# Performance work log

Measured on AMD Instinct MI355X. Metric: run time of the kernel, lower is better.

The kernel has to match this reference:

```python
import jax, jax.numpy as jnp
import numpy as np

B, P, L = 8, 196, 80
DIM1, DIM2, ATT = 2048, 300, 1024


def setup_inputs() -> dict:
    key = jax.random.key(0)
    ks = jax.random.split(key, 8)
    s1 = 1.0 / np.sqrt(DIM1)
    s2 = 1.0 / np.sqrt(DIM2)
    sa = 1.0 / np.sqrt(ATT)
    return {
        "x1": jax.random.normal(ks[0], (B, P, DIM1), jnp.float32),
        "x2": jax.random.normal(ks[1], (B, L, DIM2), jnp.float32),
        "W1": jax.random.uniform(ks[2], (ATT, DIM1), jnp.float32, -s1, s1),
        "W2": jax.random.uniform(ks[3], (ATT, DIM2), jnp.float32, -s2, s2),
        "Wh": jax.random.uniform(ks[4], (ATT, ATT), jnp.float32, -sa, sa),
        "bh": jax.random.uniform(ks[5], (ATT,), jnp.float32, -sa, sa),
        "wt": jax.random.uniform(ks[6], (ATT,), jnp.float32, -sa, sa),
        "bt": jax.random.uniform(ks[7], (), jnp.float32, -sa, sa),
    }


def reference(x1, x2, W1, W2, Wh, bh, wt, bt):
    # project: p1 (B,P,A), p2 (B,L,A)
    p1 = jnp.einsum("bpd,ad->bpa", x1, W1)
    p2 = jnp.einsum("bld,ad->bla", x2, W2)
    # broadcast bilinear + tanh: (B,L,P,A)
    h = jnp.tanh(p1[:, None, :, :] * p2[:, :, None, :])
    # hidden linear then target linear (rank-1 on last dim)
    t = jnp.einsum("blpa,ca->blpc", h, Wh) + bh
    alpha = jnp.einsum("blpc,c->blp", t, wt) + bt  # (B,L,P)
    return alpha
```

## Files before the change

### kernel.cpp

```cpp
#include <hip/hip_runtime.h>
#include <hip/hip_bf16.h>

static constexpr int kB   = 8;
static constexpr int kP   = 196;
static constexpr int kL   = 80;
static constexpr int kD1  = 2048;
static constexpr int kD2  = 300;
static constexpr int kD2p = 320;
static constexpr int kATT = 1024;
static constexpr int kM   = kB * kP;
static constexpr int kR2  = kB * kL;
static constexpr int kOut = kB * kL * kP;
static constexpr int kASplit = 16;
static constexpr int kAChunk = kATT / kASplit;
static constexpr int kLPer   = 5;

static constexpr float kTanhScale = 2.8853900817779268f;

__device__ __forceinline__ unsigned short f2bf(float x) {
    union { float f; unsigned int u; } c; c.f = x;
    unsigned int r = c.u + 0x7fffu + ((c.u >> 16) & 1u);
    return (unsigned short)(r >> 16);
}

typedef __attribute__((ext_vector_type(8))) short  bf16x8;
typedef __attribute__((ext_vector_type(4))) float  f32x4;

__device__ __forceinline__ void load_lds16(const void* g, void* l) {
    __builtin_amdgcn_global_load_lds(
        (const __attribute__((address_space(1))) void*)g,
        (__attribute__((address_space(3))) void*)l, 16, 0, 0);
}

static constexpr int kN4a = kM * kD1 / 4;
static constexpr int kN4b = kATT * kD1 / 4;
static constexpr int kN1  = kR2 * kD2p;
static constexpr int kN2  = kATT * kD2p;
static constexpr int kCastBlocks =
    (kN4a + kN4b + kN1 + kN2 + 255) / 256;

__global__ __launch_bounds__(256) void prep_kernel(
        const float* __restrict__ x1, unsigned short* __restrict__ x1b,
        const float* __restrict__ W1, unsigned short* __restrict__ W1b,
        const float* __restrict__ x2, unsigned short* __restrict__ x2b,
        const float* __restrict__ W2, unsigned short* __restrict__ W2b,
        const float* __restrict__ Wh, const float* __restrict__ wt,
        const float* __restrict__ bh, const float* __restrict__ bt,
        float* __restrict__ v, float* __restrict__ beta) {
    if (blockIdx.x >= kCastBlocks) {
        int bid = blockIdx.x - kCastBlocks;
        int ax  = bid & 3;
        int c0  = (bid >> 2) * 64;
        int a   = ax * 256 + threadIdx.x;
        float acc = 0.0f;
        #pragma unroll 8
        for (int c = c0; c < c0 + 64; ++c)
            acc = fmaf(wt[c], Wh[(size_t)c * kATT + a], acc);
        atomicAdd(&v[a], acc);
        if (ax == 0 && threadIdx.x < 64) {
            int c = c0 + threadIdx.x;
            float pb = wt[c] * bh[c];
            #pragma unroll
            for (int off = 32; off > 0; off >>= 1)
                pb += __shfl_down(pb, off, 64);
            if (threadIdx.x == 0) {
                if (c0 == 0) pb += bt[0];
                atomicAdd(beta, pb);
            }
        }
        return;
    }
    int i = blockIdx.x * 256 + threadIdx.x;
    if (i < kN4a) {
        float4 f = ((const float4*)x1)[i];
        ushort4 o = { f2bf(f.x), f2bf(f.y), f2bf(f.z), f2bf(f.w) };
        ((ushort4*)x1b)[i] = o;
    } else if ((i -= kN4a) < kN4b) {
        float4 f = ((const float4*)W1)[i];
        ushort4 o = { f2bf(f.x), f2bf(f.y), f2bf(f.z), f2bf(f.w) };
        ((ushort4*)W1b)[i] = o;
    } else if ((i -= kN4b) < kN1) {
        int r = i / kD2p, c = i - r * kD2p;
        x2b[i] = (c < kD2) ? f2bf(x2[(size_t)r * kD2 + c]) : (unsigned short)0;
    } else if ((i -= kN1) < kN2) {
        int r = i / kD2p, c = i - r * kD2p;
        W2b[i] = (c < kD2) ? f2bf(W2[(size_t)r * kD2 + c]) : (unsigned short)0;
    }
}

static constexpr int kP2Blocks = (kR2 / 64) * (kATT / 64);
static constexpr int kP1Blocks = ((kM + 63) / 64) * (kATT / 64);

__global__ __launch_bounds__(256) void gemm_all_kernel(
        const unsigned short* __restrict__ x2b, const unsigned short* __restrict__ W2b,
        float* __restrict__ p2w,
        const unsigned short* __restrict__ x1b, const unsigned short* __restrict__ W1b,
        float* __restrict__ p1w) {
    __shared__ unsigned short As[64 * 64];
    __shared__ unsigned short Bs[64 * 64];

    const unsigned short *Ab, *Bb;
    float* Co; int M, K, mx, nx; float scale;
    {
        int bid = blockIdx.x;
        if (bid < kP2Blocks) {
            Ab = x2b; Bb = W2b; Co = p2w; M = kR2; K = kD2p; scale = 1.0f;
            mx = bid % (kR2 / 64); nx = bid / (kR2 / 64);
        } else {
            int l = bid - kP2Blocks;
            Ab = x1b; Bb = W1b; Co = p1w; M = kM; K = kD1; scale = kTanhScale;
            mx = l % ((kM + 63) / 64); nx = l / ((kM + 63) / 64);
        }
    }
    const int m0   = mx * 64;
    const int n0   = nx * 64;
    const int tid  = threadIdx.x;
    const int lane = tid & 63;
    const int wv   = tid >> 6;
    const int mh   = (wv >> 1) * 32;
    const int nh   = (wv & 1) * 32;

    const int row0 = tid >> 3;
    const int row1 = row0 + 32;
    const int kx   = ((tid & 7) ^ (row0 & 7)) * 8;
    const int ar0 = min(m0 + row0, M - 1), ar1 = min(m0 + row1, M - 1);
    const int br0 = n0 + row0,             br1 = n0 + row1;

    f32x4 acc[2][2] = {};
    for (int k0 = 0; k0 < K; k0 += 64) {
        load_lds16(Ab + (size_t)ar0 * K + k0 + kx, (char*)As + tid * 16);
        load_lds16(Ab + (size_t)ar1 * K + k0 + kx, (char*)As + (tid + 256) * 16);
        load_lds16(Bb + (size_t)br0 * K + k0 + kx, (char*)Bs + tid * 16);
        load_lds16(Bb + (size_t)br1 * K + k0 + kx, (char*)Bs + (tid + 256) * 16);
        __syncthreads();

        #pragma unroll
        for (int kk = 0; kk < 2; ++kk) {
            bf16x8 af[2], bf[2];
            #pragma unroll
            for (int i = 0; i < 2; ++i) {
                int r   = mh + i * 16 + (lane & 15);
                int col = (kk * 64 + (lane >> 4) * 16) ^ ((r & 7) << 4);
                af[i] = *(const bf16x8*)((const char*)As + r * 128 + col);
            }
            #pragma unroll
            for (int j = 0; j < 2; ++j) {
                int r   = nh + j * 16 + (lane & 15);
                int col = (kk * 64 + (lane >> 4) * 16) ^ ((r & 7) << 4);
                bf[j] = *(const bf16x8*)((const char*)Bs + r * 128 + col);
            }
            #pragma unroll
            for (int i = 0; i < 2; ++i)
                #pragma unroll
                for (int j = 0; j < 2; ++j)
                    acc[i][j] = __builtin_amdgcn_mfma_f32_16x16x32_bf16(
                                    af[i], bf[j], acc[i][j], 0, 0, 0);
        }
        __syncthreads();
    }

    #pragma unroll
    for (int i = 0; i < 2; ++i)
        #pragma unroll
        for (int j = 0; j < 2; ++j)
            #pragma unroll
            for (int r = 0; r < 4; ++r) {
                int m = m0 + mh + i * 16 + (lane >> 4) * 4 + r;
                int n = n0 + nh + j * 16 + (lane & 15);
                if (m < M) Co[(size_t)m * kATT + n] = scale * acc[i][j][r];
            }
}

__global__ __launch_bounds__(256) void alpha_kernel(
        const float* __restrict__ p1, const float* __restrict__ p2,
        const float* __restrict__ v, float* __restrict__ part) {
    __shared__ float vs[kAChunk];
    __shared__ float sred;
    const int b     = blockIdx.y;
    const int as    = blockIdx.z;
    const int aBase = as * kAChunk;
    const int p0    = blockIdx.x * 16;
    const int tid   = threadIdx.x;
    const int tp    = tid & 15;
    const int lg    = tid >> 4;

    if (tid < kAChunk) vs[tid] = v[aBase + tid];
    __syncthreads();
    if (tid < 64) {
        float s = vs[tid & (kAChunk - 1)] * ((tid < kAChunk) ? 1.0f : 0.0f);
        s = vs[tid < kAChunk ? tid : 0];
        if (tid >= kAChunk) s = 0.0f;
        #pragma unroll
        for (int off = 32; off > 0; off >>= 1)
            s += __shfl_down(s, off, 64);
        if (tid == 0) sred = s;
    }
    __syncthreads();
    const float sumV = sred;

    const int p   = p0 + tp;
    const int gr1 = b * kP + min(p, kP - 1);
    const float* pu = p1 + (size_t)gr1 * kATT + aBase;
    const float* pw = p2 + ((size_t)(b * kL + lg * kLPer)) * kATT + aBase;

    float acc[kLPer] = {};
    #pragma unroll 2
    for (int a4 = 0; a4 < kAChunk / 4; ++a4) {
        float4 u  = *(const float4*)(pu + a4 * 4);
        float4 vv = *(const float4*)&vs[a4 * 4];
        #pragma unroll
        for (int j = 0; j < kLPer; ++j) {
            float4 w = *(const float4*)(pw + (size_t)j * kATT + a4 * 4);
            acc[j] = fmaf(vv.x, __builtin_amdgcn_rcpf(__builtin_amdgcn_exp2f(u.x * w.x) + 1.0f), acc[j]);
            acc[j] = fmaf(vv.y, __builtin_amdgcn_rcpf(__builtin_amdgcn_exp2f(u.y * w.y) + 1.0f), acc[j]);
            acc[j] = fmaf(vv.z, __builtin_amdgcn_rcpf(__builtin_amdgcn_exp2f(u.z * w.z) + 1.0f), acc[j]);
            acc[j] = fmaf(vv.w, __builtin_amdgcn_rcpf(__builtin_amdgcn_exp2f(u.w * w.w) + 1.0f), acc[j]);
        }
    }
    if (p < kP) {
        float* po = part + (size_t)as * kOut + ((size_t)b * kL + lg * kLPer) * kP + p;
        #pragma unroll
        for (int j = 0; j < kLPer; ++j)
            po[(size_t)j * kP] = sumV - 2.0f * acc[j];
    }
}

__global__ __launch_bounds__(256) void reduce_kernel(
        const float* __restrict__ part, const float* __restrict__ beta,
        float* __restrict__ out) {
    int i = blockIdx.x * 256 + threadIdx.x;
    if (i < kOut) {
        float s = beta[0];
        #pragma unroll
        for (int r = 0; r < kASplit; ++r)
            s += part[(size_t)r * kOut + i];
        out[i] = s;
    }
}

extern "C" void kernel_launch(void* const* d_in, const int* in_sizes, int n_in,
                              void* d_out, int out_size, void* d_ws, size_t ws_size,
                              hipStream_t stream) {
    const float* x1 = (const float*)d_in[0];
    const float* x2 = (const float*)d_in[1];
    const float* W1 = (const float*)d_in[2];
    const float* W2 = (const float*)d_in[3];
    const float* Wh = (const float*)d_in[4];
    const float* bh = (const float*)d_in[5];
    const float* wt = (const float*)d_in[6];
    const float* bt = (const float*)d_in[7];
    float* out = (float*)d_out;

    float* ws   = (float*)d_ws;
    float* v    = ws;
    float* beta = ws + 1024;
    float* p2w  = ws + 1088;
    float* p1w  = p2w + (size_t)kR2 * kATT;
    unsigned short* x1b = (unsigned short*)(p1w + (size_t)kM * kATT);
    unsigned short* W1b = x1b + (size_t)kM * kD1;
    unsigned short* x2b = W1b + (size_t)kATT * kD1;
    unsigned short* W2b = x2b + (size_t)kR2 * kD2p;
    float* part = (float*)(W2b + (size_t)kATT * kD2p);

    hipMemsetAsync(ws, 0, 1088 * sizeof(float), stream);

    prep_kernel<<<dim3(kCastBlocks + 64), 256, 0, stream>>>(
        x1, x1b, W1, W1b, x2, x2b, W2, W2b, Wh, wt, bh, bt, v, beta);
    gemm_all_kernel<<<dim3(kP2Blocks + kP1Blocks), 256, 0, stream>>>(
        x2b, W2b, p2w, x1b, W1b, p1w);
    alpha_kernel<<<dim3((kP + 15) / 16, kB, kASplit), 256, 0, stream>>>(
        p1w, p2w, v, part);
    reduce_kernel<<<dim3((kOut + 255) / 256), 256, 0, stream>>>(part, beta, out);
}
```

Baseline: 148.4 us.

## Use 128x128 split-K double-buffered P1 GEMM and atomic output accumulation

The large x1·W1 projection now uses 128x128 tiles with a 2-way K split and double-buffered LDS prefetch, writing two partial buffers that alpha_kernel sums on load. The reduce kernel and partial buffer are gone: the GEMM launch also initialises the output with beta, and alpha_kernel atomically adds its per-chunk contributions. The v/beta precompute drops the memset and atomics in favour of full per-thread loops over only 4 blocks. Trade-offs are more LDS per block, extra p1 reads in alpha, float atomic contention on the output, and a long serial loop in the v computation.

```diff
diff --git a/kernel.cpp b/kernel.cpp
--- a/kernel.cpp
+++ b/kernel.cpp
@@ -49,24 +49,21 @@
         float* __restrict__ v, float* __restrict__ beta) {
     if (blockIdx.x >= kCastBlocks) {
         int bid = blockIdx.x - kCastBlocks;
-        int ax  = bid & 3;
-        int c0  = (bid >> 2) * 64;
-        int a   = ax * 256 + threadIdx.x;
+        int a   = bid * 256 + threadIdx.x;
         float acc = 0.0f;
         #pragma unroll 8
-        for (int c = c0; c < c0 + 64; ++c)
+        for (int c = 0; c < kATT; ++c)
             acc = fmaf(wt[c], Wh[(size_t)c * kATT + a], acc);
-        atomicAdd(&v[a], acc);
-        if (ax == 0 && threadIdx.x < 64) {
-            int c = c0 + threadIdx.x;
-            float pb = wt[c] * bh[c];
+        v[a] = acc;
+        if (bid == 0 && threadIdx.x < 64) {
+            float pb = 0.0f;
+            #pragma unroll 4
+            for (int c = threadIdx.x; c < kATT; c += 64)
+                pb = fmaf(wt[c], bh[c], pb);
             #pragma unroll
             for (int off = 32; off > 0; off >>= 1)
                 pb += __shfl_down(pb, off, 64);
-            if (threadIdx.x == 0) {
-                if (c0 == 0) pb += bt[0];
-                atomicAdd(beta, pb);
-            }
+            if (threadIdx.x == 0) beta[0] = pb + bt[0];
         }
         return;
     }
@@ -88,92 +85,180 @@
     }
 }
 
-static constexpr int kP2Blocks = (kR2 / 64) * (kATT / 64);
-static constexpr int kP1Blocks = ((kM + 63) / 64) * (kATT / 64);
+static constexpr int kP1Mt      = (kM + 127) / 128;
+static constexpr int kP1Blocks  = kP1Mt * (kATT / 128) * 2;
+static constexpr int kP2Blocks  = (kR2 / 64) * (kATT / 64);
+static constexpr int kInitBlocks = (kOut + 255) / 256;
+static constexpr int kKHalf     = kD1 / 2;
 
 __global__ __launch_bounds__(256) void gemm_all_kernel(
         const unsigned short* __restrict__ x2b, const unsigned short* __restrict__ W2b,
         float* __restrict__ p2w,
         const unsigned short* __restrict__ x1b, const unsigned short* __restrict__ W1b,
-        float* __restrict__ p1w) {
-    __shared__ unsigned short As[64 * 64];
-    __shared__ unsigned short Bs[64 * 64];
-
-    const unsigned short *Ab, *Bb;
-    float* Co; int M, K, mx, nx; float scale;
-    {
-        int bid = blockIdx.x;
-        if (bid < kP2Blocks) {
-            Ab = x2b; Bb = W2b; Co = p2w; M = kR2; K = kD2p; scale = 1.0f;
-            mx = bid % (kR2 / 64); nx = bid / (kR2 / 64);
-        } else {
-            int l = bid - kP2Blocks;
-            Ab = x1b; Bb = W1b; Co = p1w; M = kM; K = kD1; scale = kTanhScale;
-            mx = l % ((kM + 63) / 64); nx = l / ((kM + 63) / 64);
-        }
-    }
-    const int m0   = mx * 64;
-    const int n0   = nx * 64;
+        float* __restrict__ p1a, float* __restrict__ p1b,
+        const float* __restrict__ beta, float* __restrict__ outp) {
+    __shared__ unsigned short As2[2][128 * 64];
+    __shared__ unsigned short Bs2[2][128 * 64];
+
+    const int bid  = blockIdx.x;
     const int tid  = threadIdx.x;
     const int lane = tid & 63;
     const int wv   = tid >> 6;
-    const int mh   = (wv >> 1) * 32;
-    const int nh   = (wv & 1) * 32;
-
-    const int row0 = tid >> 3;
-    const int row1 = row0 + 32;
-    const int kx   = ((tid & 7) ^ (row0 & 7)) * 8;
-    const int ar0 = min(m0 + row0, M - 1), ar1 = min(m0 + row1, M - 1);
-    const int br0 = n0 + row0,             br1 = n0 + row1;
-
-    f32x4 acc[2][2] = {};
-    for (int k0 = 0; k0 < K; k0 += 64) {
-        load_lds16(Ab + (size_t)ar0 * K + k0 + kx, (char*)As + tid * 16);
-        load_lds16(Ab + (size_t)ar1 * K + k0 + kx, (char*)As + (tid + 256) * 16);
-        load_lds16(Bb + (size_t)br0 * K + k0 + kx, (char*)Bs + tid * 16);
-        load_lds16(Bb + (size_t)br1 * K + k0 + kx, (char*)Bs + (tid + 256) * 16);
+
+    if (bid >= kP1Blocks + kP2Blocks) {
+        int i = (bid - kP1Blocks - kP2Blocks) * 256 + tid;
+        if (i < kOut) outp[i] = beta[0];
+        return;
+    }
+
+    if (bid < kP1Blocks) {
+        const int l  = bid;
+        const int ks = l & 1;
+        const int t  = l >> 1;
+        const int mx = t % kP1Mt, nx = t / kP1Mt;
+        const int m0 = mx * 128, n0 = nx * 128;
+        const int kBeg = ks * kKHalf;
+
+        const int srow = tid >> 3;
+        const int kx   = ((tid & 7) ^ (srow & 7)) * 8;
+        int ar[4], br[4];
+        #pragma unroll
+        for (int q = 0; q < 4; ++q) {
+            ar[q] = min(m0 + srow + q * 32, kM - 1);
+            br[q] = n0 + srow + q * 32;
+        }
+        const int wr = (wv >> 1) * 64;
+        const int wc = (wv & 1) * 64;
+
+        f32x4 acc[4][4] = {};
+
+        #pragma unroll
+        for (int q = 0; q < 4; ++q) {
+            load_lds16(x1b + (size_t)ar[q] * kD1 + kBeg + kx,
+                       (char*)As2[0] + (tid + q * 256) * 16);
+            load_lds16(W1b + (size_t)br[q] * kD1 + kBeg + kx,
+                       (char*)Bs2[0] + (tid + q * 256) * 16);
+        }
         __syncthreads();
 
-        #pragma unroll
-        for (int kk = 0; kk < 2; ++kk) {
-            bf16x8 af[2], bf[2];
-            #pragma unroll
-            for (int i = 0; i < 2; ++i) {
-                int r   = mh + i * 16 + (lane & 15);
-                int col = (kk * 64 + (lane >> 4) * 16) ^ ((r & 7) << 4);
-                af[i] = *(const bf16x8*)((const char*)As + r * 128 + col);
+        int buf = 0;
+        for (int k0 = 0; k0 < kKHalf; k0 += 64) {
+            if (k0 + 64 < kKHalf) {
+                const int kp = kBeg + k0 + 64;
+                #pragma unroll
+                for (int q = 0; q < 4; ++q) {
+                    load_lds16(x1b + (size_t)ar[q] * kD1 + kp + kx,
+                               (char*)As2[buf ^ 1] + (tid + q * 256) * 16);
+                    load_lds16(W1b + (size_t)br[q] * kD1 + kp + kx,
+                               (char*)Bs2[buf ^ 1] + (tid + q * 256) * 16);
+                }
             }
-            #pragma unroll
-            for (int j = 0; j < 2; ++j) {
-                int r   = nh + j * 16 + (lane & 15);
-                int col = (kk * 64 + (lane >> 4) * 16) ^ ((r & 7) << 4);
-                bf[j] = *(const bf16x8*)((const char*)Bs + r * 128 + col);
+            const char* Ap = (const char*)As2[buf];
+            const char* Bp = (const char*)Bs2[buf];
+            #pragma unroll
+            for (int kk = 0; kk < 2; ++kk) {
+                bf16x8 af[4], bf[4];
+                #pragma unroll
+                for (int i = 0; i < 4; ++i) {
+                    int r   = wr + i * 16 + (lane & 15);
+                    int col = (kk * 64 + (lane >> 4) * 16) ^ ((r & 7) << 4);
+                    af[i] = *(const bf16x8*)(Ap + r * 128 + col);
+                }
+                #pragma unroll
+                for (int j = 0; j < 4; ++j) {
+                    int r   = wc + j * 16 + (lane & 15);
+                    int col = (kk * 64 + (lane >> 4) * 16) ^ ((r & 7) << 4);
+                    bf[j] = *(const bf16x8*)(Bp + r * 128 + col);
+                }
+                #pragma unroll
+                for (int i = 0; i < 4; ++i)
+                    #pragma unroll
+                    for (int j = 0; j < 4; ++j)
+                        acc[i][j] = __builtin_amdgcn_mfma_f32_16x16x32_bf16(
+                                        af[i], bf[j], acc[i][j], 0, 0, 0);
             }
-            #pragma unroll
-            for (int i = 0; i < 2; ++i)
-                #pragma unroll
-                for (int j = 0; j < 2; ++j)
-                    acc[i][j] = __builtin_amdgcn_mfma_f32_16x16x32_bf16(
-                                    af[i], bf[j], acc[i][j], 0, 0, 0);
-        }
-        __syncthreads();
-    }
-
-    #pragma unroll
-    for (int i = 0; i < 2; ++i)
-        #pragma unroll
-        for (int j = 0; j < 2; ++j)
-            #pragma unroll
-            for (int r = 0; r < 4; ++r) {
-                int m = m0 + mh + i * 16 + (lane >> 4) * 4 + r;
-                int n = n0 + nh + j * 16 + (lane & 15);
-                if (m < M) Co[(size_t)m * kATT + n] = scale * acc[i][j][r];
+            __syncthreads();
+            buf ^= 1;
+        }
+
+        float* Co = ks ? p1b : p1a;
+        #pragma unroll
+        for (int i = 0; i < 4; ++i)
+            #pragma unroll
+            for (int j = 0; j < 4; ++j)
+                #pragma unroll
+                for (int r = 0; r < 4; ++r) {
+                    int m = m0 + wr + i * 16 + (lane >> 4) * 4 + r;
+                    int n = n0 + wc + j * 16 + (lane & 15);
+                    if (m < kM) Co[(size_t)m * kATT + n] = kTanhScale * acc[i][j][r];
+                }
+        return;
+    }
+
+    {
+        const int l  = bid - kP1Blocks;
+        const int mx = l % (kR2 / 64), nx = l / (kR2 / 64);
+        const int m0 = mx * 64, n0 = nx * 64;
+        unsigned short* As = As2[0];
+        unsigned short* Bs = Bs2[0];
+
+        const int mh = (wv >> 1) * 32;
+        const int nh = (wv & 1) * 32;
+        const int row0 = tid >> 3;
+        const int kx   = ((tid & 7) ^ (row0 & 7)) * 8;
+        const int ar0 = min(m0 + row0, kR2 - 1), ar1 = min(m0 + row0 + 32, kR2 - 1);
+        const int br0 = n0 + row0,               br1 = n0 + row0 + 32;
+
+        f32x4 acc[2][2] = {};
+        for (int k0 = 0; k0 < kD2p; k0 += 64) {
+            load_lds16(x2b + (size_t)ar0 * kD2p + k0 + kx, (char*)As + tid * 16);
+            load_lds16(x2b + (size_t)ar1 * kD2p + k0 + kx, (char*)As + (tid + 256) * 16);
+            load_lds16(W2b + (size_t)br0 * kD2p + k0 + kx, (char*)Bs + tid * 16);
+            load_lds16(W2b + (size_t)br1 * kD2p + k0 + kx, (char*)Bs + (tid + 256) * 16);
+            __syncthreads();
+
+            #pragma unroll
+            for (int kk = 0; kk < 2; ++kk) {
+                bf16x8 af[2], bf[2];
+                #pragma unroll
+                for (int i = 0; i < 2; ++i) {
+                    int r   = mh + i * 16 + (lane & 15);
+                    int col = (kk * 64 + (lane >> 4) * 16) ^ ((r & 7) << 4);
+                    af[i] = *(const bf16x8*)((const char*)As + r * 128 + col);
+                }
+                #pragma unroll
+                for (int j = 0; j < 2; ++j) {
+                    int r   = nh + j * 16 + (lane & 15);
+                    int col = (kk * 64 + (lane >> 4) * 16) ^ ((r & 7) << 4);
+                    bf[j] = *(const bf16x8*)((const char*)Bs + r * 128 + col);
+                }
+                #pragma unroll
+                for (int i = 0; i < 2; ++i)
+                    #pragma unroll
+                    for (int j = 0; j < 2; ++j)
+                        acc[i][j] = __builtin_amdgcn_mfma_f32_16x16x32_bf16(
+                                        af[i], bf[j], acc[i][j], 0, 0, 0);
             }
+            __syncthreads();
+        }
+
+        #pragma unroll
+        for (int i = 0; i < 2; ++i)
+            #pragma unroll
+            for (int j = 0; j < 2; ++j)
+                #pragma unroll
+                for (int r = 0; r < 4; ++r) {
+                    int m = m0 + mh + i * 16 + (lane >> 4) * 4 + r;
+                    int n = n0 + nh + j * 16 + (lane & 15);
+                    if (m < kR2) p2w[(size_t)m * kATT + n] = acc[i][j][r];
+                }
+    }
 }
 
 __global__ __launch_bounds__(256) void alpha_kernel(
-        const float* __restrict__ p1, const float* __restrict__ p2,
-        const float* __restrict__ v, float* __restrict__ part) {
+        const float* __restrict__ p1A, const float* __restrict__ p1B,
+        const float* __restrict__ p2,
+        const float* __restrict__ v, float* __restrict__ outp) {
     __shared__ float vs[kAChunk];
     __shared__ float sred;
     const int b     = blockIdx.y;
@@ -187,9 +272,7 @@
     if (tid < kAChunk) vs[tid] = v[aBase + tid];
     __syncthreads();
     if (tid < 64) {
-        float s = vs[tid & (kAChunk - 1)] * ((tid < kAChunk) ? 1.0f : 0.0f);
-        s = vs[tid < kAChunk ? tid : 0];
-        if (tid >= kAChunk) s = 0.0f;
+        float s = vs[tid];
         #pragma unroll
         for (int off = 32; off > 0; off >>= 1)
             s += __shfl_down(s, off, 64);
@@ -200,13 +283,16 @@
 
     const int p   = p0 + tp;
     const int gr1 = b * kP + min(p, kP - 1);
-    const float* pu = p1 + (size_t)gr1 * kATT + aBase;
-    const float* pw = p2 + ((size_t)(b * kL + lg * kLPer)) * kATT + aBase;
+    const float* puA = p1A + (size_t)gr1 * kATT + aBase;
+    const float* puB = p1B + (size_t)gr1 * kATT + aBase;
+    const float* pw  = p2 + ((size_t)(b * kL + lg * kLPer)) * kATT + aBase;
 
     float acc[kLPer] = {};
     #pragma unroll 2
     for (int a4 = 0; a4 < kAChunk / 4; ++a4) {
-        float4 u  = *(const float4*)(pu + a4 * 4);
+        float4 uA = *(const float4*)(puA + a4 * 4);
+        float4 uB = *(const float4*)(puB + a4 * 4);
+        float4 u  = { uA.x + uB.x, uA.y + uB.y, uA.z + uB.z, uA.w + uB.w };
         float4 vv = *(const float4*)&vs[a4 * 4];
         #pragma unroll
         for (int j = 0; j < kLPer; ++j) {
@@ -218,23 +304,10 @@
         }
     }
     if (p < kP) {
-        float* po = part + (size_t)as * kOut + ((size_t)b * kL + lg * kLPer) * kP + p;
+        float* po = outp + ((size_t)b * kL + lg * kLPer) * kP + p;
         #pragma unroll
         for (int j = 0; j < kLPer; ++j)
-            po[(size_t)j * kP] = sumV - 2.0f * acc[j];
-    }
-}
-
-__global__ __launch_bounds__(256) void reduce_kernel(
-        const float* __restrict__ part, const float* __restrict__ beta,
-        float* __restrict__ out) {
-    int i = blockIdx.x * 256 + threadIdx.x;
-    if (i < kOut) {
-        float s = beta[0];
-        #pragma unroll
-        for (int r = 0; r < kASplit; ++r)
-            s += part[(size_t)r * kOut + i];
-        out[i] = s;
+            atomicAdd(&po[(size_t)j * kP], sumV - 2.0f * acc[j]);
     }
 }
 
@@ -255,20 +328,17 @@
     float* v    = ws;
     float* beta = ws + 1024;
     float* p2w  = ws + 1088;
-    float* p1w  = p2w + (size_t)kR2 * kATT;
-    unsigned short* x1b = (unsigned short*)(p1w + (size_t)kM * kATT);
+    float* p1a  = p2w + (size_t)kR2 * kATT;
+    float* p1b  = p1a + (size_t)kM * kATT;
+    unsigned short* x1b = (unsigned short*)(p1b + (size_t)kM * kATT);
     unsigned short* W1b = x1b + (size_t)kM * kD1;
     unsigned short* x2b = W1b + (size_t)kATT * kD1;
     unsigned short* W2b = x2b + (size_t)kR2 * kD2p;
-    float* part = (float*)(W2b + (size_t)kATT * kD2p);
-
-    hipMemsetAsync(ws, 0, 1088 * sizeof(float), stream);
-
-    prep_kernel<<<dim3(kCastBlocks + 64), 256, 0, stream>>>(
+
+    prep_kernel<<<dim3(kCastBlocks + 4), 256, 0, stream>>>(
         x1, x1b, W1, W1b, x2, x2b, W2, W2b, Wh, wt, bh, bt, v, beta);
-    gemm_all_kernel<<<dim3(kP2Blocks + kP1Blocks), 256, 0, stream>>>(
-        x2b, W2b, p2w, x1b, W1b, p1w);
+    gemm_all_kernel<<<dim3(kP1Blocks + kP2Blocks + kInitBlocks), 256, 0, stream>>>(
+        x2b, W2b, p2w, x1b, W1b, p1a, p1b, beta, out);
     alpha_kernel<<<dim3((kP + 15) / 16, kB, kASplit), 256, 0, stream>>>(
-        p1w, p2w, v, part);
-    reduce_kernel<<<dim3((kOut + 255) / 256), 256, 0, stream>>>(part, beta, out);
-}
+        p1a, p1b, p2w, v, out);
+}
```

Result: slower. 197.5 us (+33.1%).
